# Optimization experiments

Hardware: AMD Instinct MI355X
Metric: run time of the kernel (lower is better)

The kernel has to match this reference:

```python
import jax, jax.numpy as jnp
import numpy as np

N = 100000
E = 300000
IN_C = 256
HID = 256   # 2 * out_channels
OUT_C = 128


def setup_inputs() -> dict:
    key = jax.random.key(0)
    k1, k2, k3, k4, k5 = jax.random.split(key, 5)
    x = jax.random.normal(k1, (N, IN_C), dtype=jnp.float32)
    edge_index = jax.random.randint(k2, (2, E), 0, N, dtype=jnp.int64)
    # Glorot-style init scale for GEMM weights
    W1 = jax.random.normal(k3, (IN_C, HID), dtype=jnp.float32) * (1.0 / np.sqrt(IN_C))
    b1 = jnp.zeros((HID,), dtype=jnp.float32)
    W2 = jax.random.normal(k4, (HID, OUT_C), dtype=jnp.float32) * (1.0 / np.sqrt(HID))
    b2 = jnp.zeros((OUT_C,), dtype=jnp.float32)
    return {"x": x, "edge_index": edge_index, "W1": W1, "b1": b1, "W2": W2, "b2": b2}


def _gcn_conv(x, W, b, src, dst, norm, n_nodes):
    # x: [N, Fin] -> transform then gather-scale-scatter aggregate
    h = x @ W                                   # [N, Fout]
    msgs = h[src] * norm[:, None]               # [E+N, Fout] (includes self-loops)
    out = jax.ops.segment_sum(msgs, dst, num_segments=n_nodes)
    return out + b


def _gcn_norm(edge_index, n_nodes):
    # add self-loops, compute symmetric deg^-1/2 normalization (PyG GCNConv default)
    loops = jnp.arange(n_nodes, dtype=edge_index.dtype)
    src = jnp.concatenate([edge_index[0], loops])
    dst = jnp.concatenate([edge_index[1], loops])
    deg = jax.ops.segment_sum(jnp.ones_like(dst, dtype=jnp.float32), dst, num_segments=n_nodes)
    dinv = jnp.where(deg > 0, jax.lax.rsqrt(deg), 0.0)
    norm = dinv[src] * dinv[dst]                # [E+N]
    return src, dst, norm


def reference(x, edge_index, W1, b1, W2, b2):
    n_nodes = x.shape[0]
    src, dst, norm = _gcn_norm(edge_index, n_nodes)
    h = _gcn_conv(x, W1, b1, src, dst, norm, n_nodes)
    h = jax.nn.relu(h)
    # dropout is identity in eval mode (reference baseline runs deterministic eval)
    return _gcn_conv(h, W2, b2, src, dst, norm, n_nodes)
```

## Files before the change

kernel.cpp:

```cpp
#include <hip/hip_runtime.h>
#include <stdint.h>

#define IN_C  256
#define HID   256
#define OUT_C 128
#define SCAN_BS 1024

typedef __bf16 bf16x8 __attribute__((ext_vector_type(8)));
typedef float  f32x4  __attribute__((ext_vector_type(4)));
typedef unsigned short u16x8 __attribute__((ext_vector_type(8)));
typedef unsigned short u16x4 __attribute__((ext_vector_type(4)));
typedef unsigned short u16x2 __attribute__((ext_vector_type(2)));
typedef unsigned int u32;

static __device__ __forceinline__ unsigned short f2b(float f) {
    union { float f; uint32_t u; } v; v.f = f;
    uint32_t r = v.u + 0x7fffu + ((v.u >> 16) & 1u);
    return (unsigned short)(r >> 16);
}
static __device__ __forceinline__ float b2f(unsigned short b) {
    union { uint32_t u; float f; } v; v.u = ((uint32_t)b) << 16;
    return v.f;
}

typedef __attribute__((address_space(1))) const u32 gas_u32;
typedef __attribute__((address_space(3))) u32 las_u32;
static __device__ __forceinline__ void gld16(const void* g, void* l) {
    __builtin_amdgcn_global_load_lds((gas_u32*)g, (las_u32*)l, 16, 0, 0);
}
static __device__ __forceinline__ u32 cvtpk(float lo, float hi) {
    u32 r;
    asm("v_cvt_pk_bf16_f32 %0, %1, %2" : "=v"(r) : "v"(lo), "v"(hi));
    return r;
}

__global__ void k_zero_i(int* __restrict__ p, int n) {
    int i = blockIdx.x * blockDim.x + threadIdx.x;
    if (i < n) p[i] = 0;
}

__global__ void k_count(const int* __restrict__ dst, int* __restrict__ cnt, int e) {
    int i = blockIdx.x * blockDim.x + threadIdx.x;
    if (i < e) atomicAdd(&cnt[dst[i]], 1);
}

__global__ __launch_bounds__(SCAN_BS) void k_scan_block(
    const int* __restrict__ cnt, int* __restrict__ rs, int* __restrict__ bsum, int n) {
    __shared__ int s[SCAN_BS];
    const int tid = threadIdx.x;
    const int i = blockIdx.x * SCAN_BS + tid;
    int v = (i < n) ? cnt[i] + 1 : 0;
    s[tid] = v;
    __syncthreads();
    for (int off = 1; off < SCAN_BS; off <<= 1) {
        int t = (tid >= off) ? s[tid - off] : 0;
        __syncthreads();
        s[tid] += t;
        __syncthreads();
    }
    if (i < n) rs[i] = s[tid] - v;
    if (tid == SCAN_BS - 1) bsum[blockIdx.x] = s[tid];
}

__global__ void k_scan_sums(int* __restrict__ bsum, int nb) {
    __shared__ int s[128];
    const int tid = threadIdx.x;
    int v = (tid < nb) ? bsum[tid] : 0;
    s[tid] = v;
    __syncthreads();
    for (int off = 1; off < 128; off <<= 1) {
        int t = (tid >= off) ? s[tid - off] : 0;
        __syncthreads();
        s[tid] += t;
        __syncthreads();
    }
    if (tid < nb) bsum[tid] = s[tid] - v;
}

__global__ void k_scan_add(int* __restrict__ rs, int* __restrict__ cur,
                           const int* __restrict__ bsum, const int* __restrict__ cnt,
                           float* __restrict__ dinv, int2* __restrict__ csrw, int n) {
    int i = blockIdx.x * blockDim.x + threadIdx.x;
    if (i < n) {
        int v = rs[i] + bsum[i >> 10];
        rs[i] = v;
        cur[i] = v + 1;
        float dp1 = (float)(cnt[i] + 1);
        dinv[i] = rsqrtf(dp1);
        csrw[v] = make_int2(i, __float_as_int(1.0f / dp1));
    }
}

__global__ void k_fill(const int* __restrict__ src, const int* __restrict__ dst,
                       const float* __restrict__ dinv,
                       int* __restrict__ cur, int2* __restrict__ csrw, int e) {
    int i = blockIdx.x * blockDim.x + threadIdx.x;
    if (i < e) {
        int s = src[i], d = dst[i];
        int p = atomicAdd(&cur[d], 1);
        csrw[p] = make_int2(s, __float_as_int(dinv[s] * dinv[d]));
    }
}

__global__ void k_prep(const float* __restrict__ W1, const float* __restrict__ W2,
                       unsigned short* __restrict__ W1T, unsigned short* __restrict__ W2T) {
    int i = blockIdx.x * blockDim.x + threadIdx.x;
    if (i < 65536) W1T[i] = f2b(W1[(i & 255) * HID + (i >> 8)]);
    if (i < 32768) W2T[i] = f2b(W2[(i & 255) * OUT_C + (i >> 8)]);
}

__global__ __launch_bounds__(256) void k_gemm1(
    const float* __restrict__ x, const unsigned short* __restrict__ W1T,
    unsigned short* __restrict__ t1, int n) {
    __shared__ __align__(16) float Af[128 * 32];
    __shared__ __align__(16) unsigned short Bs[128 * 32];
    const int tid = threadIdx.x;
    const int bm = blockIdx.x >> 1, bn = blockIdx.x & 1;
    const int row0 = bm * 128, col0 = bn * 128;
    const int wid = tid >> 6, lane = tid & 63;
    const int wm = wid >> 1, wn = wid & 1;
    const int lrow = lane & 15, lgrp = lane >> 4;

    f32x4 acc[4][4];
    #pragma unroll
    for (int i = 0; i < 4; ++i)
        #pragma unroll
        for (int j = 0; j < 4; ++j)
            acc[i][j] = (f32x4){0.f, 0.f, 0.f, 0.f};

    for (int kt = 0; kt < 8; ++kt) {
        #pragma unroll
        for (int i = 0; i < 4; ++i) {
            int s = tid + 256 * i;
            int r = s >> 3, c = s & 7;
            int grow = row0 + r; if (grow > n - 1) grow = n - 1;
            gld16(x + (size_t)grow * IN_C + kt * 32 + ((c ^ (r & 7)) << 2), Af + s * 4);
        }
        #pragma unroll
        for (int i = 0; i < 2; ++i) {
            int s = tid + 256 * i;
            int nn = s >> 2, c = s & 3;
            gld16(W1T + (size_t)(col0 + nn) * 256 + kt * 32 + c * 8, Bs + s * 8);
        }
        __syncthreads();

        bf16x8 av[4], bv[4];
        #pragma unroll
        for (int mf = 0; mf < 4; ++mf) {
            int r = wm * 64 + mf * 16 + lrow;
            f32x4 l = *(const f32x4*)&Af[r * 32 + (((2 * lgrp) ^ (r & 7)) << 2)];
            f32x4 h = *(const f32x4*)&Af[r * 32 + (((2 * lgrp + 1) ^ (r & 7)) << 2)];
            union { u32 w[4]; bf16x8 b; } u;
            u.w[0] = cvtpk(l[0], l[1]); u.w[1] = cvtpk(l[2], l[3]);
            u.w[2] = cvtpk(h[0], h[1]); u.w[3] = cvtpk(h[2], h[3]);
            av[mf] = u.b;
        }
        #pragma unroll
        for (int nf = 0; nf < 4; ++nf) {
            int cc = wn * 64 + nf * 16 + lrow;
            bv[nf] = *(const bf16x8*)&Bs[cc * 32 + lgrp * 8];
        }
        #pragma unroll
        for (int mf = 0; mf < 4; ++mf)
            #pragma unroll
            for (int nf = 0; nf < 4; ++nf)
                acc[mf][nf] = __builtin_amdgcn_mfma_f32_16x16x32_bf16(
                    av[mf], bv[nf], acc[mf][nf], 0, 0, 0);
        __syncthreads();
    }
    #pragma unroll
    for (int mf = 0; mf < 4; ++mf)
        #pragma unroll
        for (int j = 0; j < 4; ++j) {
            int grow = row0 + wm * 64 + mf * 16 + lgrp * 4 + j;
            if (grow < n) {
                #pragma unroll
                for (int nf = 0; nf < 4; ++nf) {
                    int col = col0 + wn * 64 + nf * 16 + lrow;
                    t1[(size_t)grow * HID + col] = f2b(acc[mf][nf][j]);
                }
            }
        }
}

__global__ __launch_bounds__(256) void k_agg1(
    const unsigned short* __restrict__ t1, const int* __restrict__ rs,
    const int* __restrict__ cnt, const int2* __restrict__ csrw,
    const float* __restrict__ b1, unsigned short* __restrict__ out1, int n) {
    const int w = blockIdx.x * 4 + (threadIdx.x >> 6);
    const int nodeA = w * 2, nodeB = w * 2 + 1;
    if (nodeA >= n) return;
    const bool hasB = (nodeB < n);
    const int lane = threadIdx.x & 63;
    const int ch = lane * 4;
    const int begA = rs[nodeA], mA = cnt[nodeA] + 1;
    int begB = 0, mB = 0;
    if (hasB) { begB = rs[nodeB]; mB = cnt[nodeB] + 1; }
    float a0 = 0.f, a1 = 0.f, a2 = 0.f, a3 = 0.f;
    float c0 = 0.f, c1 = 0.f, c2 = 0.f, c3 = 0.f;
    const int mmax = mA > mB ? mA : mB;
    for (int j = 0; j < mmax; ++j) {
        if (j < mA) {
            int2 p = csrw[begA + j];
            float wA = __int_as_float(p.y);
            u16x4 u = *(const u16x4*)&t1[(size_t)p.x * HID + ch];
            a0 += b2f(u[0]) * wA; a1 += b2f(u[1]) * wA;
            a2 += b2f(u[2]) * wA; a3 += b2f(u[3]) * wA;
        }
        if (j < mB) {
            int2 p = csrw[begB + j];
            float wB = __int_as_float(p.y);
            u16x4 u = *(const u16x4*)&t1[(size_t)p.x * HID + ch];
            c0 += b2f(u[0]) * wB; c1 += b2f(u[1]) * wB;
            c2 += b2f(u[2]) * wB; c3 += b2f(u[3]) * wB;
        }
    }
    float4 bb = *(const float4*)(b1 + ch);
    u16x4 o;
    o[0] = f2b(fmaxf(a0 + bb.x, 0.f));
    o[1] = f2b(fmaxf(a1 + bb.y, 0.f));
    o[2] = f2b(fmaxf(a2 + bb.z, 0.f));
    o[3] = f2b(fmaxf(a3 + bb.w, 0.f));
    *(u16x4*)&out1[(size_t)nodeA * HID + ch] = o;
    if (hasB) {
        u16x4 q;
        q[0] = f2b(fmaxf(c0 + bb.x, 0.f));
        q[1] = f2b(fmaxf(c1 + bb.y, 0.f));
        q[2] = f2b(fmaxf(c2 + bb.z, 0.f));
        q[3] = f2b(fmaxf(c3 + bb.w, 0.f));
        *(u16x4*)&out1[(size_t)nodeB * HID + ch] = q;
    }
}

__global__ __launch_bounds__(256) void k_gemm2(
    const unsigned short* __restrict__ out1, const unsigned short* __restrict__ W2T,
    unsigned short* __restrict__ t2, int n) {
    __shared__ __align__(16) unsigned short Ah[128 * 32];
    __shared__ __align__(16) unsigned short Bs[128 * 32];
    const int tid = threadIdx.x;
    const int row0 = blockIdx.x * 128;
    const int wid = tid >> 6, lane = tid & 63;
    const int wm = wid >> 1, wn = wid & 1;
    const int lrow = lane & 15, lgrp = lane >> 4;

    f32x4 acc[4][4];
    #pragma unroll
    for (int i = 0; i < 4; ++i)
        #pragma unroll
        for (int j = 0; j < 4; ++j)
            acc[i][j] = (f32x4){0.f, 0.f, 0.f, 0.f};

    for (int kt = 0; kt < 8; ++kt) {
        #pragma unroll
        for (int i = 0; i < 2; ++i) {
            int s = tid + 256 * i;
            int r = s >> 2, c = s & 3;
            int grow = row0 + r; if (grow > n - 1) grow = n - 1;
            gld16(out1 + (size_t)grow * HID + kt * 32 + c * 8, Ah + s * 8);
        }
        #pragma unroll
        for (int i = 0; i < 2; ++i) {
            int s = tid + 256 * i;
            int nn = s >> 2, c = s & 3;
            gld16(W2T + (size_t)nn * 256 + kt * 32 + c * 8, Bs + s * 8);
        }
        __syncthreads();

        bf16x8 av[4], bv[4];
        #pragma unroll
        for (int mf = 0; mf < 4; ++mf) {
            int r = wm * 64 + mf * 16 + lrow;
            av[mf] = *(const bf16x8*)&Ah[r * 32 + lgrp * 8];
        }
        #pragma unroll
        for (int nf = 0; nf < 4; ++nf) {
            int cc = wn * 64 + nf * 16 + lrow;
            bv[nf] = *(const bf16x8*)&Bs[cc * 32 + lgrp * 8];
        }
        #pragma unroll
        for (int mf = 0; mf < 4; ++mf)
            #pragma unroll
            for (int nf = 0; nf < 4; ++nf)
                acc[mf][nf] = __builtin_amdgcn_mfma_f32_16x16x32_bf16(
                    av[mf], bv[nf], acc[mf][nf], 0, 0, 0);
        __syncthreads();
    }
    #pragma unroll
    for (int mf = 0; mf < 4; ++mf)
        #pragma unroll
        for (int j = 0; j < 4; ++j) {
            int grow = row0 + wm * 64 + mf * 16 + lgrp * 4 + j;
            if (grow < n) {
                #pragma unroll
                for (int nf = 0; nf < 4; ++nf) {
                    int col = wn * 64 + nf * 16 + lrow;
                    t2[(size_t)grow * OUT_C + col] = f2b(acc[mf][nf][j]);
                }
            }
        }
}

__global__ __launch_bounds__(256) void k_agg2(
    const unsigned short* __restrict__ t2, const int* __restrict__ rs,
    const int* __restrict__ cnt, const int2* __restrict__ csrw,
    const float* __restrict__ b2, float* __restrict__ out, int n) {
    const int w = blockIdx.x * 4 + (threadIdx.x >> 6);
    const int nodeA = w * 2, nodeB = w * 2 + 1;
    if (nodeA >= n) return;
    const bool hasB = (nodeB < n);
    const int lane = threadIdx.x & 63;
    const int ch = lane * 2;
    const int begA = rs[nodeA], mA = cnt[nodeA] + 1;
    int begB = 0, mB = 0;
    if (hasB) { begB = rs[nodeB]; mB = cnt[nodeB] + 1; }
    float a0 = 0.f, a1 = 0.f, c0 = 0.f, c1 = 0.f;
    const int mmax = mA > mB ? mA : mB;
    for (int j = 0; j < mmax; ++j) {
        if (j < mA) {
            int2 p = csrw[begA + j];
            float wA = __int_as_float(p.y);
            u16x2 u = *(const u16x2*)&t2[(size_t)p.x * OUT_C + ch];
            a0 += b2f(u[0]) * wA; a1 += b2f(u[1]) * wA;
        }
        if (j < mB) {
            int2 p = csrw[begB + j];
            float wB = __int_as_float(p.y);
            u16x2 u = *(const u16x2*)&t2[(size_t)p.x * OUT_C + ch];
            c0 += b2f(u[0]) * wB; c1 += b2f(u[1]) * wB;
        }
    }
    float2 bb = *(const float2*)(b2 + ch);
    *(float2*)&out[(size_t)nodeA * OUT_C + ch] = make_float2(a0 + bb.x, a1 + bb.y);
    if (hasB)
        *(float2*)&out[(size_t)nodeB * OUT_C + ch] = make_float2(c0 + bb.x, c1 + bb.y);
}

extern "C" void kernel_launch(void* const* d_in, const int* in_sizes, int n_in,
                              void* d_out, int out_size, void* d_ws, size_t ws_size,
                              hipStream_t stream) {
    const float* x  = (const float*)d_in[0];
    const int*   ei = (const int*)d_in[1];
    const float* W1 = (const float*)d_in[2];
    const float* b1 = (const float*)d_in[3];
    const float* W2 = (const float*)d_in[4];
    const float* b2 = (const float*)d_in[5];
    float* out = (float*)d_out;

    const int n = in_sizes[0] / IN_C;
    const int e = in_sizes[1] / 2;
    const int* src = ei;
    const int* dst = ei + e;

    int*   cnt  = (int*)d_ws;
    int*   rs   = cnt + n;
    int*   cur  = rs + n;
    int*   bsum = cur + n;
    float* dinv = (float*)(bsum + 128);
    int2*  csrw = (int2*)(dinv + n);
    unsigned short* W1T = (unsigned short*)(csrw + (size_t)e + n);
    unsigned short* W2T = W1T + 65536;
    unsigned short* t1  = W2T + 32768;
    unsigned short* out1 = t1 + (size_t)n * HID;
    unsigned short* t2  = t1;

    const int nb = (n + SCAN_BS - 1) / SCAN_BS;

    k_zero_i<<<(n + 255) / 256, 256, 0, stream>>>(cnt, n);
    k_count<<<(e + 255) / 256, 256, 0, stream>>>(dst, cnt, e);
    k_scan_block<<<nb, SCAN_BS, 0, stream>>>(cnt, rs, bsum, n);
    k_scan_sums<<<1, 128, 0, stream>>>(bsum, nb);
    k_scan_add<<<(n + 255) / 256, 256, 0, stream>>>(rs, cur, bsum, cnt, dinv, csrw, n);
    k_fill<<<(e + 255) / 256, 256, 0, stream>>>(src, dst, dinv, cur, csrw, e);
    k_prep<<<256, 256, 0, stream>>>(W1, W2, W1T, W2T);

    const int mb = (n + 127) / 128;
    k_gemm1<<<mb * 2, 256, 0, stream>>>(x, W1T, t1, n);
    const int aggblk = (n + 7) / 8;
    k_agg1<<<aggblk, 256, 0, stream>>>(t1, rs, cnt, csrw, b1, out1, n);
    k_gemm2<<<mb, 256, 0, stream>>>(out1, W2T, t2, n);
    k_agg2<<<aggblk, 256, 0, stream>>>(t2, rs, cnt, csrw, b2, out, n);
}
```

Measured before the change: 216.9 us.

## Rewrite GEMMs as persistent kernels with register-resident weights and direct A loads

Both GEMM kernels become persistent grids of 512-thread blocks. Each wave keeps its slice of the transposed bf16 weight matrix in registers for the whole kernel and loops over 16-row tiles, loading A rows straight from global memory into registers with no LDS staging or barriers. This removes the shared-memory round trip and the syncthreads, and stops the weight tiles from being reloaded in every block. In exchange it uses many more VGPRs, which may lower occupancy, and the per-lane A loads are strided and less coalesced.

```diff
diff --git a/kernel.cpp b/kernel.cpp
--- a/kernel.cpp
+++ b/kernel.cpp
@@ -21,12 +21,6 @@
 static __device__ __forceinline__ float b2f(unsigned short b) {
     union { uint32_t u; float f; } v; v.u = ((uint32_t)b) << 16;
     return v.f;
-}
-
-typedef __attribute__((address_space(1))) const u32 gas_u32;
-typedef __attribute__((address_space(3))) u32 las_u32;
-static __device__ __forceinline__ void gld16(const void* g, void* l) {
-    __builtin_amdgcn_global_load_lds((gas_u32*)g, (las_u32*)l, 16, 0, 0);
 }
 static __device__ __forceinline__ u32 cvtpk(float lo, float hi) {
     u32 r;
@@ -109,78 +103,57 @@
     if (i < 32768) W2T[i] = f2b(W2[(i & 255) * OUT_C + (i >> 8)]);
 }
 
-__global__ __launch_bounds__(256) void k_gemm1(
+__global__ __launch_bounds__(512) void k_gemm1(
     const float* __restrict__ x, const unsigned short* __restrict__ W1T,
-    unsigned short* __restrict__ t1, int n) {
-    __shared__ __align__(16) float Af[128 * 32];
-    __shared__ __align__(16) unsigned short Bs[128 * 32];
+    unsigned short* __restrict__ t1, int n, int ntiles) {
     const int tid = threadIdx.x;
-    const int bm = blockIdx.x >> 1, bn = blockIdx.x & 1;
-    const int row0 = bm * 128, col0 = bn * 128;
     const int wid = tid >> 6, lane = tid & 63;
-    const int wm = wid >> 1, wn = wid & 1;
+    const int wc0 = (wid & 3) * 64;
+    const int rg  = wid >> 2;
     const int lrow = lane & 15, lgrp = lane >> 4;
 
-    f32x4 acc[4][4];
+    bf16x8 b[4][8];
     #pragma unroll
-    for (int i = 0; i < 4; ++i)
-        #pragma unroll
-        for (int j = 0; j < 4; ++j)
-            acc[i][j] = (f32x4){0.f, 0.f, 0.f, 0.f};
-
-    for (int kt = 0; kt < 8; ++kt) {
-        #pragma unroll
-        for (int i = 0; i < 4; ++i) {
-            int s = tid + 256 * i;
-            int r = s >> 3, c = s & 7;
-            int grow = row0 + r; if (grow > n - 1) grow = n - 1;
-            gld16(x + (size_t)grow * IN_C + kt * 32 + ((c ^ (r & 7)) << 2), Af + s * 4);
-        }
-        #pragma unroll
-        for (int i = 0; i < 2; ++i) {
-            int s = tid + 256 * i;
-            int nn = s >> 2, c = s & 3;
-            gld16(W1T + (size_t)(col0 + nn) * 256 + kt * 32 + c * 8, Bs + s * 8);
-        }
-        __syncthreads();
-
-        bf16x8 av[4], bv[4];
-        #pragma unroll
-        for (int mf = 0; mf < 4; ++mf) {
-            int r = wm * 64 + mf * 16 + lrow;
-            f32x4 l = *(const f32x4*)&Af[r * 32 + (((2 * lgrp) ^ (r & 7)) << 2)];
-            f32x4 h = *(const f32x4*)&Af[r * 32 + (((2 * lgrp + 1) ^ (r & 7)) << 2)];
-            union { u32 w[4]; bf16x8 b; } u;
-            u.w[0] = cvtpk(l[0], l[1]); u.w[1] = cvtpk(l[2], l[3]);
-            u.w[2] = cvtpk(h[0], h[1]); u.w[3] = cvtpk(h[2], h[3]);
-            av[mf] = u.b;
-        }
-        #pragma unroll
-        for (int nf = 0; nf < 4; ++nf) {
-            int cc = wn * 64 + nf * 16 + lrow;
-            bv[nf] = *(const bf16x8*)&Bs[cc * 32 + lgrp * 8];
-        }
-        #pragma unroll
-        for (int mf = 0; mf < 4; ++mf)
+    for (int nf = 0; nf < 4; ++nf)
+        #pragma unroll
+        for (int kk = 0; kk < 8; ++kk)
+            b[nf][kk] = *(const bf16x8*)&W1T[(size_t)(wc0 + nf * 16 + lrow) * 256 + kk * 32 + lgrp * 8];
+
+    for (int t = blockIdx.x * 2 + rg; t < ntiles; t += 512) {
+        int ar = t * 16 + lrow; if (ar > n - 1) ar = n - 1;
+        const float* ap = x + (size_t)ar * 256 + lgrp * 8;
+        f32x4 lo[8], hi[8];
+        #pragma unroll
+        for (int kk = 0; kk < 8; ++kk) {
+            lo[kk] = *(const f32x4*)(ap + kk * 32);
+            hi[kk] = *(const f32x4*)(ap + kk * 32 + 4);
+        }
+        union { u32 w[4]; bf16x8 v; } a[8];
+        #pragma unroll
+        for (int kk = 0; kk < 8; ++kk) {
+            a[kk].w[0] = cvtpk(lo[kk][0], lo[kk][1]);
+            a[kk].w[1] = cvtpk(lo[kk][2], lo[kk][3]);
+            a[kk].w[2] = cvtpk(hi[kk][0], hi[kk][1]);
+            a[kk].w[3] = cvtpk(hi[kk][2], hi[kk][3]);
+        }
+        f32x4 acc[4];
+        #pragma unroll
+        for (int nf = 0; nf < 4; ++nf) acc[nf] = (f32x4){0.f, 0.f, 0.f, 0.f};
+        #pragma unroll
+        for (int kk = 0; kk < 8; ++kk)
             #pragma unroll
             for (int nf = 0; nf < 4; ++nf)
-                acc[mf][nf] = __builtin_amdgcn_mfma_f32_16x16x32_bf16(
-                    av[mf], bv[nf], acc[mf][nf], 0, 0, 0);
-        __syncthreads();
-    }
-    #pragma unroll
-    for (int mf = 0; mf < 4; ++mf)
-        #pragma unroll
-        for (int j = 0; j < 4; ++j) {
-            int grow = row0 + wm * 64 + mf * 16 + lgrp * 4 + j;
-            if (grow < n) {
-                #pragma unroll
-                for (int nf = 0; nf < 4; ++nf) {
-                    int col = col0 + wn * 64 + nf * 16 + lrow;
-                    t1[(size_t)grow * HID + col] = f2b(acc[mf][nf][j]);
-                }
+                acc[nf] = __builtin_amdgcn_mfma_f32_16x16x32_bf16(
+                    a[kk].v, b[nf][kk], acc[nf], 0, 0, 0);
+        unsigned short* op = t1 + ((size_t)t * 16 + lgrp * 4) * HID + wc0 + lrow;
+        #pragma unroll
+        for (int nf = 0; nf < 4; ++nf)
+            #pragma unroll
+            for (int j = 0; j < 4; ++j) {
+                int r = t * 16 + lgrp * 4 + j;
+                if (r < n) op[(size_t)j * HID + nf * 16] = f2b(acc[nf][j]);
             }
-        }
+    }
 }
 
 __global__ __launch_bounds__(256) void k_agg1(
@@ -232,72 +205,47 @@
     }
 }
 
-__global__ __launch_bounds__(256) void k_gemm2(
+__global__ __launch_bounds__(512) void k_gemm2(
     const unsigned short* __restrict__ out1, const unsigned short* __restrict__ W2T,
-    unsigned short* __restrict__ t2, int n) {
-    __shared__ __align__(16) unsigned short Ah[128 * 32];
-    __shared__ __align__(16) unsigned short Bs[128 * 32];
+    unsigned short* __restrict__ t2, int n, int ntiles) {
     const int tid = threadIdx.x;
-    const int row0 = blockIdx.x * 128;
     const int wid = tid >> 6, lane = tid & 63;
-    const int wm = wid >> 1, wn = wid & 1;
+    const int wc0 = (wid & 3) * 32;
+    const int rg  = wid >> 2;
     const int lrow = lane & 15, lgrp = lane >> 4;
 
-    f32x4 acc[4][4];
+    bf16x8 b[2][8];
     #pragma unroll
-    for (int i = 0; i < 4; ++i)
-        #pragma unroll
-        for (int j = 0; j < 4; ++j)
-            acc[i][j] = (f32x4){0.f, 0.f, 0.f, 0.f};
-
-    for (int kt = 0; kt < 8; ++kt) {
-        #pragma unroll
-        for (int i = 0; i < 2; ++i) {
-            int s = tid + 256 * i;
-            int r = s >> 2, c = s & 3;
-            int grow = row0 + r; if (grow > n - 1) grow = n - 1;
-            gld16(out1 + (size_t)grow * HID + kt * 32 + c * 8, Ah + s * 8);
-        }
-        #pragma unroll
-        for (int i = 0; i < 2; ++i) {
-            int s = tid + 256 * i;
-            int nn = s >> 2, c = s & 3;
-            gld16(W2T + (size_t)nn * 256 + kt * 32 + c * 8, Bs + s * 8);
-        }
-        __syncthreads();
-
-        bf16x8 av[4], bv[4];
-        #pragma unroll
-        for (int mf = 0; mf < 4; ++mf) {
-            int r = wm * 64 + mf * 16 + lrow;
-            av[mf] = *(const bf16x8*)&Ah[r * 32 + lgrp * 8];
-        }
-        #pragma unroll
-        for (int nf = 0; nf < 4; ++nf) {
-            int cc = wn * 64 + nf * 16 + lrow;
-            bv[nf] = *(const bf16x8*)&Bs[cc * 32 + lgrp * 8];
-        }
-        #pragma unroll
-        for (int mf = 0; mf < 4; ++mf)
+    for (int nf = 0; nf < 2; ++nf)
+        #pragma unroll
+        for (int kk = 0; kk < 8; ++kk)
+            b[nf][kk] = *(const bf16x8*)&W2T[(size_t)(wc0 + nf * 16 + lrow) * 256 + kk * 32 + lgrp * 8];
+
+    for (int t = blockIdx.x * 2 + rg; t < ntiles; t += 1024) {
+        int ar = t * 16 + lrow; if (ar > n - 1) ar = n - 1;
+        const unsigned short* ap = out1 + (size_t)ar * HID + lgrp * 8;
+        bf16x8 a[8];
+        #pragma unroll
+        for (int kk = 0; kk < 8; ++kk)
+            a[kk] = *(const bf16x8*)(ap + kk * 32);
+        f32x4 acc[2];
+        acc[0] = (f32x4){0.f, 0.f, 0.f, 0.f};
+        acc[1] = (f32x4){0.f, 0.f, 0.f, 0.f};
+        #pragma unroll
+        for (int kk = 0; kk < 8; ++kk)
             #pragma unroll
-            for (int nf = 0; nf < 4; ++nf)
-                acc[mf][nf] = __builtin_amdgcn_mfma_f32_16x16x32_bf16(
-                    av[mf], bv[nf], acc[mf][nf], 0, 0, 0);
-        __syncthreads();
-    }
-    #pragma unroll
-    for (int mf = 0; mf < 4; ++mf)
-        #pragma unroll
-        for (int j = 0; j < 4; ++j) {
-            int grow = row0 + wm * 64 + mf * 16 + lgrp * 4 + j;
-            if (grow < n) {
-                #pragma unroll
-                for (int nf = 0; nf < 4; ++nf) {
-                    int col = wn * 64 + nf * 16 + lrow;
-                    t2[(size_t)grow * OUT_C + col] = f2b(acc[mf][nf][j]);
-                }
+            for (int nf = 0; nf < 2; ++nf)
+                acc[nf] = __builtin_amdgcn_mfma_f32_16x16x32_bf16(
+                    a[kk], b[nf][kk], acc[nf], 0, 0, 0);
+        unsigned short* op = t2 + ((size_t)t * 16 + lgrp * 4) * OUT_C + wc0 + lrow;
+        #pragma unroll
+        for (int nf = 0; nf < 2; ++nf)
+            #pragma unroll
+            for (int j = 0; j < 4; ++j) {
+                int r = t * 16 + lgrp * 4 + j;
+                if (r < n) op[(size_t)j * OUT_C + nf * 16] = f2b(acc[nf][j]);
             }
-        }
+    }
 }
 
 __global__ __launch_bounds__(256) void k_agg2(
@@ -373,10 +321,10 @@
     k_fill<<<(e + 255) / 256, 256, 0, stream>>>(src, dst, dinv, cur, csrw, e);
     k_prep<<<256, 256, 0, stream>>>(W1, W2, W1T, W2T);
 
-    const int mb = (n + 127) / 128;
-    k_gemm1<<<mb * 2, 256, 0, stream>>>(x, W1T, t1, n);
+    const int ntiles = (n + 15) / 16;
+    k_gemm1<<<256, 512, 0, stream>>>(x, W1T, t1, n, ntiles);
     const int aggblk = (n + 7) / 8;
     k_agg1<<<aggblk, 256, 0, stream>>>(t1, rs, cnt, csrw, b1, out1, n);
-    k_gemm2<<<mb, 256, 0, stream>>>(out1, W2T, t2, n);
+    k_gemm2<<<512, 512, 0, stream>>>(out1, W2T, t2, n, ntiles);
     k_agg2<<<aggblk, 256, 0, stream>>>(t2, rs, cnt, csrw, b2, out, n);
 }
```

New measurement: 264.8 us. +22.1%, slower.
